# Kernel optimization log

Hardware: AMD Instinct MI355X
Metric: run time of the kernel (lower is better)

Reference implementation:

```python
import jax, jax.numpy as jnp
import numpy as np

IN_F, OUT_F = 4096, 4096
IN_Q, OUT_Q = IN_F // 4, OUT_F // 4


def setup_inputs() -> dict:
    key = jax.random.key(0)
    kx, kr, ki, kj, kk = jax.random.split(key, 5)
    std = 1.0 / np.sqrt(IN_F)
    x = jax.random.normal(kx, (4, 2048, IN_F), dtype=jnp.float32)
    Wr = std * jax.random.normal(kr, (OUT_Q, IN_Q), dtype=jnp.float32)
    Wi = std * jax.random.normal(ki, (OUT_Q, IN_Q), dtype=jnp.float32)
    Wj = std * jax.random.normal(kj, (OUT_Q, IN_Q), dtype=jnp.float32)
    Wk = std * jax.random.normal(kk, (OUT_Q, IN_Q), dtype=jnp.float32)
    bias = jnp.zeros((OUT_F,), dtype=jnp.float32)
    return {"x": x, "Wr": Wr, "Wi": Wi, "Wj": Wj, "Wk": Wk, "bias": bias}


def _hamilton_block(Wr, Wi, Wj, Wk):
    # Assemble the structured [4*out_q, 4*in_q] Hamilton block weight so the
    # whole op is ONE large GEMM instead of 16 small ones (same math).
    row_r = jnp.concatenate([Wr, -Wi, -Wj, -Wk], axis=1)
    row_i = jnp.concatenate([Wi,  Wr,  Wk, -Wj], axis=1)
    row_j = jnp.concatenate([Wj, -Wk,  Wr,  Wi], axis=1)
    row_k = jnp.concatenate([Wk,  Wj, -Wi,  Wr], axis=1)
    return jnp.concatenate([row_r, row_i, row_j, row_k], axis=0)  # [OUT_F, IN_F]


def reference(x, Wr, Wi, Wj, Wk, bias):
    W = _hamilton_block(Wr, Wi, Wj, Wk)
    # x: [B, S, IN_F] @ W.T -> [B, S, OUT_F]
    out = jnp.einsum('bsf,of->bso', x, W) + bias
    return out
```

## Files before the change

### kernel.cpp

```cpp
#include <hip/hip_runtime.h>
#include <hip/hip_bf16.h>


#define M_DIM 8192
#define N_DIM 4096
#define K_DIM 4096
#define BK 64
#define NT (K_DIM / BK)

typedef __attribute__((ext_vector_type(8))) short bf16x8;
typedef __attribute__((ext_vector_type(4))) float f32x4;
typedef __attribute__((ext_vector_type(8))) unsigned short ushort8;

static __device__ __forceinline__ unsigned short f2bf(float f) {
    unsigned int u = __float_as_uint(f);
    return (unsigned short)((u + 0x7fffu + ((u >> 16) & 1u)) >> 16);
}
static __device__ __forceinline__ unsigned short f2bf_sgn(float f, unsigned int sg) {
    unsigned int u = __float_as_uint(f) ^ sg;
    return (unsigned short)((u + 0x7fffu + ((u >> 16) & 1u)) >> 16);
}

__global__ __launch_bounds__(256) void cvt_x_kernel(const float* __restrict__ x,
                                                    unsigned short* __restrict__ xb) {
    int i = (blockIdx.x * 256 + threadIdx.x) * 8;
    f32x4 a = __builtin_nontemporal_load((const f32x4*)(x + i));
    f32x4 b = __builtin_nontemporal_load((const f32x4*)(x + i + 4));
    ushort8 o;
    o[0] = f2bf(a[0]); o[1] = f2bf(a[1]); o[2] = f2bf(a[2]); o[3] = f2bf(a[3]);
    o[4] = f2bf(b[0]); o[5] = f2bf(b[1]); o[6] = f2bf(b[2]); o[7] = f2bf(b[3]);
    *(ushort8*)(xb + i) = o;
}

__global__ __launch_bounds__(256) void prep_w_kernel(const float* __restrict__ Wr,
    const float* __restrict__ Wi, const float* __restrict__ Wj,
    const float* __restrict__ Wk, unsigned short* __restrict__ wb) {
    int row = blockIdx.x >> 1;
    int col = ((blockIdx.x & 1) * 256 + threadIdx.x) * 8;
    int p = row >> 10, q = col >> 10;
    int ci = p ^ q;
    const float* src = (ci == 0) ? Wr : (ci == 1) ? Wi : (ci == 2) ? Wj : Wk;
    unsigned int sg = ((0x428Eu >> (p * 4 + q)) & 1u) << 31;
    int so = (row & 1023) * 1024 + (col & 1023);
    f32x4 a = *(const f32x4*)(src + so);
    f32x4 b = *(const f32x4*)(src + so + 4);
    ushort8 o;
    o[0] = f2bf_sgn(a[0], sg); o[1] = f2bf_sgn(a[1], sg);
    o[2] = f2bf_sgn(a[2], sg); o[3] = f2bf_sgn(a[3], sg);
    o[4] = f2bf_sgn(b[0], sg); o[5] = f2bf_sgn(b[1], sg);
    o[6] = f2bf_sgn(b[2], sg); o[7] = f2bf_sgn(b[3], sg);
    *(ushort8*)(wb + row * 4096 + col) = o;
}

#define GLD16(gp, lp) __builtin_amdgcn_global_load_lds( \
    (const __attribute__((address_space(1))) void*)(gp), \
    (__attribute__((address_space(3))) void*)(lp), 16, 0, 0)

#define BAR() do { asm volatile("" ::: "memory"); \
                   __builtin_amdgcn_s_barrier(); \
                   asm volatile("" ::: "memory"); } while (0)
#define VM(n) asm volatile("s_waitcnt vmcnt(" #n ")" ::: "memory")

static __device__ __forceinline__ f32x4 MF(bf16x8 a, bf16x8 b, f32x4 c) {
    return __builtin_amdgcn_mfma_f32_16x16x32_bf16(a, b, c, 0, 0, 0);
}

__global__ __launch_bounds__(1024, 4) void qgemm_bf16(
    const unsigned short* __restrict__ A, const unsigned short* __restrict__ B,
    const float* __restrict__ bias, float* __restrict__ out)
{
    __shared__ __align__(16) unsigned short Lsh[2][2][256 * 64];

    int bid = blockIdx.x;
    int cpx = gridDim.x >> 3;
    int wg  = (bid & 7) * cpx + (bid >> 3);
    int brow = (wg >> 4) * 256;
    int bcol = (wg & 15) * 256;

    int tid   = threadIdx.x;
    int lane  = tid & 63;
    int wid   = tid >> 6;
    int wm    = wid >> 2;
    int wn    = wid & 3;
    int fr    = lane & 15;
    int fslot = lane >> 4;
    unsigned e = (unsigned)(fr & 7);

    const unsigned short* Ag = A + (size_t)brow * K_DIM;
    const unsigned short* Bg = B + (size_t)bcol * K_DIM;
    const char* LshB = (const char*)&Lsh[0][0][0];

    unsigned oA0 = (unsigned)wm * 8192u + (unsigned)fr * 128u
                 + ((((unsigned)fslot) ^ e) << 4);
    unsigned oA1 = oA0 ^ 64u;
    unsigned oB0 = 0x8000u + (unsigned)wn * 8192u + (unsigned)fr * 128u
                 + ((((unsigned)fslot) ^ e) << 4);
    unsigned oB1 = oB0 ^ 64u;

    f32x4 acc[4][4] = {};

    auto stage = [&](int buf, int ab, int t) {
        const unsigned short* g = (ab ? Bg : Ag) + t * BK;
        unsigned short* l = &Lsh[buf][ab][0];
        #pragma unroll
        for (int i = 0; i < 2; ++i) {
            int c = i * 1024 + tid;
            int r = c >> 3, s = c & 7;
            GLD16(g + (size_t)r * K_DIM + ((s ^ (r & 7)) << 3), l + (c << 3));
        }
    };
    auto RD = [&](unsigned off) -> bf16x8 {
        return *(const bf16x8*)(LshB + off);
    };

#define CLUSTER(mi)                                                           \
    do {                                                                      \
        bf16x8 a0 = RD(oA0 + (mi) * 2048u), a1 = RD(oA1 + (mi) * 2048u);      \
        __builtin_amdgcn_s_setprio(1);                                        \
        _Pragma("unroll")                                                     \
        for (int ni = 0; ni < 4; ++ni) acc[mi][ni] = MF(a0, bf0[ni], acc[mi][ni]); \
        _Pragma("unroll")                                                     \
        for (int ni = 0; ni < 4; ++ni) acc[mi][ni] = MF(a1, bf1[ni], acc[mi][ni]); \
        __builtin_amdgcn_s_setprio(0);                                        \
    } while (0)

    bf16x8 bf0[4], bf1[4];

    stage(0, 0, 0); stage(0, 1, 0); stage(1, 1, 1);
    VM(2); BAR();

    for (int t = 0; t < NT; ++t) {
        int buf = t & 1;

        if (t + 1 < NT) stage(buf ^ 1, 0, t + 1);
        #pragma unroll
        for (int ni = 0; ni < 4; ++ni) {
            bf0[ni] = RD(oB0 + (unsigned)(ni * 2048));
            bf1[ni] = RD(oB1 + (unsigned)(ni * 2048));
        }
        CLUSTER(0);
        BAR();

        if (t + 2 < NT) stage(buf, 1, t + 2);
        CLUSTER(1);
        CLUSTER(2);
        CLUSTER(3);

        if (t < NT - 2) { VM(2); } else { VM(0); }
        BAR();
        oA0 ^= 0x10000u; oA1 ^= 0x10000u; oB0 ^= 0x10000u; oB1 ^= 0x10000u;
    }
#undef CLUSTER

    int cr = (lane >> 4) << 2;
    int cc = lane & 15;
    #pragma unroll
    for (int ni = 0; ni < 4; ++ni) {
        int col = bcol + wn * 64 + ni * 16 + cc;
        float bv = bias[col];
        #pragma unroll
        for (int mi = 0; mi < 4; ++mi) {
            int r0 = brow + wm * 64 + mi * 16 + cr;
            #pragma unroll
            for (int r = 0; r < 4; ++r)
                __builtin_nontemporal_store(acc[mi][ni][r] + bv,
                                            &out[(size_t)(r0 + r) * N_DIM + col]);
        }
    }
}

#define FBM 128
#define FBN 128
#define FBK 64
__global__ __launch_bounds__(256) void qgemm_fb(const float* __restrict__ x,
    const float* __restrict__ Wr, const float* __restrict__ Wi,
    const float* __restrict__ Wj, const float* __restrict__ Wk,
    const float* __restrict__ bias, float* __restrict__ out)
{
    __shared__ unsigned short As[FBM * FBK];
    __shared__ unsigned short Bs[FBN * FBK];

    int bid = blockIdx.x;
    int cpx = gridDim.x >> 3;
    int wg = (bid & 7) * cpx + (bid >> 3);
    int brow = (wg >> 5) * FBM;
    int bcol = (wg & 31) * FBN;

    int tid = threadIdx.x;
    int lane = tid & 63;
    int wv = tid >> 6;
    int wm = (wv >> 1) << 6;
    int wn = (wv & 1) << 6;
    int fr = lane & 15;
    int fk = (lane >> 4) << 3;

    int p = bcol >> 10;
    f32x4 acc[4][4] = {};

    for (int kt = 0; kt < K_DIM / FBK; ++kt) {
        int k0 = kt * FBK;
        int q = k0 >> 10;
        int ci = p ^ q;
        const float* wsrc = (ci == 0) ? Wr : (ci == 1) ? Wi : (ci == 2) ? Wj : Wk;
        unsigned int sg = ((0x428Eu >> (p * 4 + q)) & 1u) << 31;

        __syncthreads();
        #pragma unroll
        for (int i = 0; i < 4; ++i) {
            int c = i * 256 + tid;
            int row = c >> 3, colo = (c & 7) << 3;
            const float* s = x + (size_t)(brow + row) * K_DIM + k0 + colo;
            float4 a = *(const float4*)s;
            float4 b = *(const float4*)(s + 4);
            ushort8 o;
            o[0] = f2bf(a.x); o[1] = f2bf(a.y); o[2] = f2bf(a.z); o[3] = f2bf(a.w);
            o[4] = f2bf(b.x); o[5] = f2bf(b.y); o[6] = f2bf(b.z); o[7] = f2bf(b.w);
            *(ushort8*)(&As[c << 3]) = o;
        }
        #pragma unroll
        for (int i = 0; i < 4; ++i) {
            int c = i * 256 + tid;
            int row = c >> 3, colo = (c & 7) << 3;
            const float* s = wsrc + ((bcol + row) & 1023) * 1024 + ((k0 + colo) & 1023);
            float4 a = *(const float4*)s;
            float4 b = *(const float4*)(s + 4);
            ushort8 o;
            o[0] = f2bf_sgn(a.x, sg); o[1] = f2bf_sgn(a.y, sg);
            o[2] = f2bf_sgn(a.z, sg); o[3] = f2bf_sgn(a.w, sg);
            o[4] = f2bf_sgn(b.x, sg); o[5] = f2bf_sgn(b.y, sg);
            o[6] = f2bf_sgn(b.z, sg); o[7] = f2bf_sgn(b.w, sg);
            *(ushort8*)(&Bs[c << 3]) = o;
        }
        __syncthreads();

        #pragma unroll
        for (int ks = 0; ks < 2; ++ks) {
            bf16x8 af[4], bfr[4];
            #pragma unroll
            for (int m = 0; m < 4; ++m)
                af[m] = *(const bf16x8*)(&As[(wm + m * 16 + fr) * FBK + ks * 32 + fk]);
            #pragma unroll
            for (int n = 0; n < 4; ++n)
                bfr[n] = *(const bf16x8*)(&Bs[(wn + n * 16 + fr) * FBK + ks * 32 + fk]);
            #pragma unroll
            for (int m = 0; m < 4; ++m)
                #pragma unroll
                for (int n = 0; n < 4; ++n)
                    acc[m][n] = __builtin_amdgcn_mfma_f32_16x16x32_bf16(
                        af[m], bfr[n], acc[m][n], 0, 0, 0);
        }
    }

    int cr = (lane >> 4) << 2;
    int cc = lane & 15;
    #pragma unroll
    for (int n = 0; n < 4; ++n) {
        int col = bcol + wn + n * 16 + cc;
        float bv = bias[col];
        #pragma unroll
        for (int m = 0; m < 4; ++m) {
            int r0 = brow + wm + m * 16 + cr;
            #pragma unroll
            for (int r = 0; r < 4; ++r)
                out[(size_t)(r0 + r) * N_DIM + col] = acc[m][n][r] + bv;
        }
    }
}

extern "C" void kernel_launch(void* const* d_in, const int* in_sizes, int n_in,
                              void* d_out, int out_size, void* d_ws, size_t ws_size,
                              hipStream_t stream) {
    const float* x    = (const float*)d_in[0];
    const float* Wr   = (const float*)d_in[1];
    const float* Wi   = (const float*)d_in[2];
    const float* Wj   = (const float*)d_in[3];
    const float* Wk   = (const float*)d_in[4];
    const float* bias = (const float*)d_in[5];
    float* out = (float*)d_out;

    const size_t xb_bytes = (size_t)M_DIM * K_DIM * 2;
    const size_t wb_bytes = (size_t)N_DIM * K_DIM * 2;

    if (ws_size >= xb_bytes + wb_bytes) {
        unsigned short* xb = (unsigned short*)d_ws;
        unsigned short* wb = (unsigned short*)((char*)d_ws + xb_bytes);
        cvt_x_kernel<<<(M_DIM * K_DIM) / 2048, 256, 0, stream>>>(x, xb);
        prep_w_kernel<<<N_DIM * 2, 256, 0, stream>>>(Wr, Wi, Wj, Wk, wb);
        const int n_blocks = (M_DIM / 256) * (N_DIM / 256);
        qgemm_bf16<<<n_blocks, 1024, 0, stream>>>(xb, wb, bias, out);
    } else {
        const int n_blocks = (M_DIM / FBM) * (N_DIM / FBN);
        qgemm_fb<<<n_blocks, 256, 0, stream>>>(x, Wr, Wi, Wj, Wk, bias, out);
    }
}
```

Measured before the change: 274.4 us.

## Restructure bf16 GEMM to 8 waves with 32x32x16 MFMA and k-slab LDS layout

Rewrites the main GEMM kernel to use 512 threads (8 waves, 2x4), each computing a 128x64 sub-tile with 32x32x16 bf16 MFMAs instead of 16x16x32. The LDS layout changes to k-slab-major staging with fixed offsets, and fragments are fetched through inline-asm ds_read_b128 with immediate offsets. A software-pipelined lgkmcnt schedule overlaps LDS reads with MFMAs. This raises per-wave data reuse and cuts LDS read traffic per FLOP. In exchange, A and B now share one double-buffered stage with a full vmcnt(0) wait each iteration, which may expose global-load latency, and the unswizzled layout risks LDS bank conflicts.

```diff
diff --git a/kernel.cpp b/kernel.cpp
--- a/kernel.cpp
+++ b/kernel.cpp
@@ -10,6 +10,7 @@
 
 typedef __attribute__((ext_vector_type(8))) short bf16x8;
 typedef __attribute__((ext_vector_type(4))) float f32x4;
+typedef __attribute__((ext_vector_type(16))) float f32x16;
 typedef __attribute__((ext_vector_type(8))) unsigned short ushort8;
 
 static __device__ __forceinline__ unsigned short f2bf(float f) {
@@ -59,17 +60,38 @@
 #define BAR() do { asm volatile("" ::: "memory"); \
                    __builtin_amdgcn_s_barrier(); \
                    asm volatile("" ::: "memory"); } while (0)
-#define VM(n) asm volatile("s_waitcnt vmcnt(" #n ")" ::: "memory")
-
-static __device__ __forceinline__ f32x4 MF(bf16x8 a, bf16x8 b, f32x4 c) {
-    return __builtin_amdgcn_mfma_f32_16x16x32_bf16(a, b, c, 0, 0, 0);
-}
-
-__global__ __launch_bounds__(1024, 4) void qgemm_bf16(
+#define VM0() asm volatile("s_waitcnt vmcnt(0)" ::: "memory")
+#define SB()  __builtin_amdgcn_sched_barrier(0)
+#define LGKM(n) do { asm volatile("s_waitcnt lgkmcnt(" #n ")" ::: "memory"); SB(); } while (0)
+
+#define DSR(dst, addr, imm) \
+    asm volatile("ds_read_b128 %0, %1 offset:" imm : "=v"(dst) : "v"(addr))
+
+#define MF32(a, b, c) __builtin_amdgcn_mfma_f32_32x32x16_bf16(a, b, c, 0, 0, 0)
+
+#define DECL6(F) bf16x8 F##a0, F##a1, F##a2, F##a3, F##b0, F##b1
+#define RD6(F, A0, A1, A2, A3, B0, B1) do { \
+    DSR(F##a0, vA, A0); DSR(F##a1, vA, A1); DSR(F##a2, vA, A2); DSR(F##a3, vA, A3); \
+    DSR(F##b0, vB, B0); DSR(F##b1, vB, B1); } while (0)
+
+#define MFMA8(F) do { \
+    __builtin_amdgcn_s_setprio(1); \
+    acc[0][0] = MF32(F##a0, F##b0, acc[0][0]); \
+    acc[0][1] = MF32(F##a0, F##b1, acc[0][1]); \
+    acc[1][0] = MF32(F##a1, F##b0, acc[1][0]); \
+    acc[1][1] = MF32(F##a1, F##b1, acc[1][1]); \
+    acc[2][0] = MF32(F##a2, F##b0, acc[2][0]); \
+    acc[2][1] = MF32(F##a2, F##b1, acc[2][1]); \
+    acc[3][0] = MF32(F##a3, F##b0, acc[3][0]); \
+    acc[3][1] = MF32(F##a3, F##b1, acc[3][1]); \
+    __builtin_amdgcn_s_setprio(0); \
+} while (0)
+
+__global__ __launch_bounds__(512, 2) void qgemm_bf16(
     const unsigned short* __restrict__ A, const unsigned short* __restrict__ B,
     const float* __restrict__ bias, float* __restrict__ out)
 {
-    __shared__ __align__(16) unsigned short Lsh[2][2][256 * 64];
+    __shared__ __align__(16) unsigned short Lsh[65536];
 
     int bid = blockIdx.x;
     int cpx = gridDim.x >> 3;
@@ -77,94 +99,80 @@
     int brow = (wg >> 4) * 256;
     int bcol = (wg & 15) * 256;
 
-    int tid   = threadIdx.x;
-    int lane  = tid & 63;
-    int wid   = tid >> 6;
-    int wm    = wid >> 2;
-    int wn    = wid & 3;
-    int fr    = lane & 15;
-    int fslot = lane >> 4;
-    unsigned e = (unsigned)(fr & 7);
+    int tid  = threadIdx.x;
+    int lane = tid & 63;
+    int wid  = tid >> 6;
+    int wm   = wid >> 2;
+    int wn   = wid & 3;
+    int l31  = lane & 31;
+    int hi   = lane >> 5;
 
     const unsigned short* Ag = A + (size_t)brow * K_DIM;
     const unsigned short* Bg = B + (size_t)bcol * K_DIM;
-    const char* LshB = (const char*)&Lsh[0][0][0];
-
-    unsigned oA0 = (unsigned)wm * 8192u + (unsigned)fr * 128u
-                 + ((((unsigned)fslot) ^ e) << 4);
-    unsigned oA1 = oA0 ^ 64u;
-    unsigned oB0 = 0x8000u + (unsigned)wn * 8192u + (unsigned)fr * 128u
-                 + ((((unsigned)fslot) ^ e) << 4);
-    unsigned oB1 = oB0 ^ 64u;
-
-    f32x4 acc[4][4] = {};
-
-    auto stage = [&](int buf, int ab, int t) {
-        const unsigned short* g = (ab ? Bg : Ag) + t * BK;
-        unsigned short* l = &Lsh[buf][ab][0];
-        #pragma unroll
-        for (int i = 0; i < 2; ++i) {
-            int c = i * 1024 + tid;
-            int r = c >> 3, s = c & 7;
-            GLD16(g + (size_t)r * K_DIM + ((s ^ (r & 7)) << 3), l + (c << 3));
-        }
+
+    unsigned lds0 = (unsigned)(size_t)(__attribute__((address_space(3))) void*)Lsh;
+    unsigned vA = lds0 + (unsigned)(wm * 4096 + l31 * 32 + hi * 16);
+    unsigned vB = lds0 + 32768u + (unsigned)(wn * 2048 + l31 * 32 + hi * 16);
+
+    int soff[4];
+    #pragma unroll
+    for (int i = 0; i < 4; ++i) {
+        int c = i * 512 + tid;
+        soff[i] = ((c >> 1) & 255) * 4096 + (c >> 9) * 16 + (c & 1) * 8;
+    }
+
+    f32x16 acc[4][2] = {};
+
+    auto STAGE = [&](int buf, int t) {
+        const unsigned short* ga = Ag + t * BK;
+        const unsigned short* gb = Bg + t * BK;
+        char* l = (char*)Lsh + buf * 65536;
+        #pragma unroll
+        for (int i = 0; i < 4; ++i)
+            GLD16(ga + soff[i], l + (i * 512 + tid) * 16);
+        #pragma unroll
+        for (int i = 0; i < 4; ++i)
+            GLD16(gb + soff[i], l + 32768 + (i * 512 + tid) * 16);
     };
-    auto RD = [&](unsigned off) -> bf16x8 {
-        return *(const bf16x8*)(LshB + off);
-    };
-
-#define CLUSTER(mi)                                                           \
-    do {                                                                      \
-        bf16x8 a0 = RD(oA0 + (mi) * 2048u), a1 = RD(oA1 + (mi) * 2048u);      \
-        __builtin_amdgcn_s_setprio(1);                                        \
-        _Pragma("unroll")                                                     \
-        for (int ni = 0; ni < 4; ++ni) acc[mi][ni] = MF(a0, bf0[ni], acc[mi][ni]); \
-        _Pragma("unroll")                                                     \
-        for (int ni = 0; ni < 4; ++ni) acc[mi][ni] = MF(a1, bf1[ni], acc[mi][ni]); \
-        __builtin_amdgcn_s_setprio(0);                                        \
-    } while (0)
-
-    bf16x8 bf0[4], bf1[4];
-
-    stage(0, 0, 0); stage(0, 1, 0); stage(1, 1, 1);
-    VM(2); BAR();
+
+    STAGE(0, 0);
+    VM0(); BAR();
 
     for (int t = 0; t < NT; ++t) {
-        int buf = t & 1;
-
-        if (t + 1 < NT) stage(buf ^ 1, 0, t + 1);
-        #pragma unroll
-        for (int ni = 0; ni < 4; ++ni) {
-            bf0[ni] = RD(oB0 + (unsigned)(ni * 2048));
-            bf1[ni] = RD(oB1 + (unsigned)(ni * 2048));
-        }
-        CLUSTER(0);
+        if (t + 1 < NT) STAGE((t & 1) ^ 1, t + 1);
+
+        DECL6(f0); DECL6(f1); DECL6(f2); DECL6(f3);
+        RD6(f0, "0", "1024", "2048", "3072", "0", "1024");
+        RD6(f1, "8192", "9216", "10240", "11264", "8192", "9216");
+        LGKM(6);
+        MFMA8(f0);
+        RD6(f2, "16384", "17408", "18432", "19456", "16384", "17408");
+        LGKM(6);
+        MFMA8(f1);
+        RD6(f3, "24576", "25600", "26624", "27648", "24576", "25600");
+        LGKM(6);
+        MFMA8(f2);
+        LGKM(0);
+        MFMA8(f3);
+
+        VM0();
         BAR();
-
-        if (t + 2 < NT) stage(buf, 1, t + 2);
-        CLUSTER(1);
-        CLUSTER(2);
-        CLUSTER(3);
-
-        if (t < NT - 2) { VM(2); } else { VM(0); }
-        BAR();
-        oA0 ^= 0x10000u; oA1 ^= 0x10000u; oB0 ^= 0x10000u; oB1 ^= 0x10000u;
-    }
-#undef CLUSTER
-
-    int cr = (lane >> 4) << 2;
-    int cc = lane & 15;
+        vA ^= 0x10000u; vB ^= 0x10000u;
+    }
+
     #pragma unroll
-    for (int ni = 0; ni < 4; ++ni) {
-        int col = bcol + wn * 64 + ni * 16 + cc;
+    for (int ni = 0; ni < 2; ++ni) {
+        int col = bcol + wn * 64 + ni * 32 + l31;
         float bv = bias[col];
         #pragma unroll
         for (int mi = 0; mi < 4; ++mi) {
-            int r0 = brow + wm * 64 + mi * 16 + cr;
-            #pragma unroll
-            for (int r = 0; r < 4; ++r)
+            int r0 = brow + wm * 128 + mi * 32 + 4 * hi;
+            #pragma unroll
+            for (int r = 0; r < 16; ++r) {
+                int row = r0 + (r & 3) + 8 * (r >> 2);
                 __builtin_nontemporal_store(acc[mi][ni][r] + bv,
-                                            &out[(size_t)(r0 + r) * N_DIM + col]);
+                                            &out[(size_t)row * N_DIM + col]);
+            }
         }
     }
 }
@@ -287,7 +295,7 @@
         cvt_x_kernel<<<(M_DIM * K_DIM) / 2048, 256, 0, stream>>>(x, xb);
         prep_w_kernel<<<N_DIM * 2, 256, 0, stream>>>(Wr, Wi, Wj, Wk, wb);
         const int n_blocks = (M_DIM / 256) * (N_DIM / 256);
-        qgemm_bf16<<<n_blocks, 1024, 0, stream>>>(xb, wb, bias, out);
+        qgemm_bf16<<<n_blocks, 512, 0, stream>>>(xb, wb, bias, out);
     } else {
         const int n_blocks = (M_DIM / FBM) * (N_DIM / FBN);
         qgemm_fb<<<n_blocks, 256, 0, stream>>>(x, Wr, Wi, Wj, Wk, bias, out);
```

Measured after the change: 311.0 us. +13.3%, slower.

## Restructure bf16 GEMM to 8 waves with 128x64 warp tiles and phased ping-pong pipeline

Applied to the files above, without the earlier changes.

The 256x256 GEMM tile is now computed by 512 threads (8 waves) instead of 1024, so each wave owns a 128x64 sub-tile with 32 accumulators. That doubles the MFMA work per LDS read of B. The main loop is unrolled by two K-steps into explicit phases. Each phase issues inline-asm ds_reads, splits global->LDS staging across the phases, and uses barriers, lgkmcnt/vmcnt waits and sched_barriers to interleave loads with MFMA clusters. The intent is more register-level reuse and finer overlap of memory with compute. The costs are higher register pressure, lower occupancy and more fragile manual scheduling.

```diff
diff --git a/kernel.cpp b/kernel.cpp
--- a/kernel.cpp
+++ b/kernel.cpp
@@ -7,6 +7,7 @@
 #define K_DIM 4096
 #define BK 64
 #define NT (K_DIM / BK)
+#define NIT (NT / 2)
 
 typedef __attribute__((ext_vector_type(8))) short bf16x8;
 typedef __attribute__((ext_vector_type(4))) float f32x4;
@@ -56,20 +57,47 @@
     (const __attribute__((address_space(1))) void*)(gp), \
     (__attribute__((address_space(3))) void*)(lp), 16, 0, 0)
 
-#define BAR() do { asm volatile("" ::: "memory"); \
-                   __builtin_amdgcn_s_barrier(); \
-                   asm volatile("" ::: "memory"); } while (0)
-#define VM(n) asm volatile("s_waitcnt vmcnt(" #n ")" ::: "memory")
-
-static __device__ __forceinline__ f32x4 MF(bf16x8 a, bf16x8 b, f32x4 c) {
-    return __builtin_amdgcn_mfma_f32_16x16x32_bf16(a, b, c, 0, 0, 0);
-}
-
-__global__ __launch_bounds__(1024, 4) void qgemm_bf16(
+#define SB()  __builtin_amdgcn_sched_barrier(0)
+#define DSR(dst, addr, imm) \
+    asm volatile("ds_read_b128 %0, %1 offset:" imm : "=v"(dst) : "v"(addr))
+#define MF(a, b, c) __builtin_amdgcn_mfma_f32_16x16x32_bf16(a, b, c, 0, 0, 0)
+
+#define RDB(B0, B1) do { \
+    DSR(b0k0, B0, "0"); DSR(b1k0, B0, "2048"); \
+    DSR(b2k0, B0, "4096"); DSR(b3k0, B0, "6144"); \
+    DSR(b0k1, B1, "0"); DSR(b1k1, B1, "2048"); \
+    DSR(b2k1, B1, "4096"); DSR(b3k1, B1, "6144"); } while (0)
+
+#define APHASE(A0, A1, I0, I1, ML, MH, WAITS, ...) do { \
+    bf16x8 xk0l, xk0h, xk1l, xk1h; \
+    DSR(xk0l, A0, I0); DSR(xk0h, A0, I1); \
+    DSR(xk1l, A1, I0); DSR(xk1h, A1, I1); \
+    __VA_ARGS__; \
+    __builtin_amdgcn_s_barrier(); \
+    asm volatile("s_waitcnt lgkmcnt(0)" ::: "memory"); SB(); \
+    __builtin_amdgcn_s_setprio(1); \
+    acc[ML][0] = MF(xk0l, b0k0, acc[ML][0]); acc[ML][1] = MF(xk0l, b1k0, acc[ML][1]); \
+    acc[ML][2] = MF(xk0l, b2k0, acc[ML][2]); acc[ML][3] = MF(xk0l, b3k0, acc[ML][3]); \
+    acc[MH][0] = MF(xk0h, b0k0, acc[MH][0]); acc[MH][1] = MF(xk0h, b1k0, acc[MH][1]); \
+    acc[MH][2] = MF(xk0h, b2k0, acc[MH][2]); acc[MH][3] = MF(xk0h, b3k0, acc[MH][3]); \
+    acc[ML][0] = MF(xk1l, b0k1, acc[ML][0]); acc[ML][1] = MF(xk1l, b1k1, acc[ML][1]); \
+    acc[ML][2] = MF(xk1l, b2k1, acc[ML][2]); acc[ML][3] = MF(xk1l, b3k1, acc[ML][3]); \
+    acc[MH][0] = MF(xk1h, b0k1, acc[MH][0]); acc[MH][1] = MF(xk1h, b1k1, acc[MH][1]); \
+    acc[MH][2] = MF(xk1h, b2k1, acc[MH][2]); acc[MH][3] = MF(xk1h, b3k1, acc[MH][3]); \
+    __builtin_amdgcn_s_setprio(0); \
+    WAITS; \
+    __builtin_amdgcn_s_barrier(); \
+} while (0)
+
+#define LGKM8() asm volatile("s_waitcnt lgkmcnt(8)" ::: "memory")
+#define VMW(n)  asm volatile("s_waitcnt vmcnt(" #n ")" ::: "memory")
+#define NOOP()  do {} while (0)
+
+__global__ __launch_bounds__(512, 2) void qgemm_bf16(
     const unsigned short* __restrict__ A, const unsigned short* __restrict__ B,
     const float* __restrict__ bias, float* __restrict__ out)
 {
-    __shared__ __align__(16) unsigned short Lsh[2][2][256 * 64];
+    __shared__ __align__(16) unsigned short Lsh[2][2][2][128 * 64];
 
     int bid = blockIdx.x;
     int cpx = gridDim.x >> 3;
@@ -80,7 +108,7 @@
     int tid   = threadIdx.x;
     int lane  = tid & 63;
     int wid   = tid >> 6;
-    int wm    = wid >> 2;
+    int hA    = wid >> 2;
     int wn    = wid & 3;
     int fr    = lane & 15;
     int fslot = lane >> 4;
@@ -88,69 +116,73 @@
 
     const unsigned short* Ag = A + (size_t)brow * K_DIM;
     const unsigned short* Bg = B + (size_t)bcol * K_DIM;
-    const char* LshB = (const char*)&Lsh[0][0][0];
-
-    unsigned oA0 = (unsigned)wm * 8192u + (unsigned)fr * 128u
-                 + ((((unsigned)fslot) ^ e) << 4);
-    unsigned oA1 = oA0 ^ 64u;
-    unsigned oB0 = 0x8000u + (unsigned)wn * 8192u + (unsigned)fr * 128u
-                 + ((((unsigned)fslot) ^ e) << 4);
-    unsigned oB1 = oB0 ^ 64u;
-
-    f32x4 acc[4][4] = {};
-
-    auto stage = [&](int buf, int ab, int t) {
-        const unsigned short* g = (ab ? Bg : Ag) + t * BK;
-        unsigned short* l = &Lsh[buf][ab][0];
-        #pragma unroll
-        for (int i = 0; i < 2; ++i) {
-            int c = i * 1024 + tid;
-            int r = c >> 3, s = c & 7;
-            GLD16(g + (size_t)r * K_DIM + ((s ^ (r & 7)) << 3), l + (c << 3));
-        }
+
+    unsigned lds0 = (unsigned)(size_t)(__attribute__((address_space(3))) void*)Lsh;
+    unsigned inrow = (((unsigned)fslot ^ e) << 4);
+    unsigned vA0e = lds0 + (unsigned)(hA * 16384 + fr * 128) + inrow;
+    unsigned vA1e = vA0e ^ 64u;
+    unsigned vA0o = vA0e + 65536u, vA1o = vA1e + 65536u;
+    unsigned vB0e = lds0 + 32768u
+                  + (unsigned)((wn >> 1) * 16384 + ((wn & 1) * 64 + fr) * 128) + inrow;
+    unsigned vB1e = vB0e ^ 64u;
+    unsigned vB0o = vB0e + 65536u, vB1o = vB1e + 65536u;
+
+    int soff0 = (tid >> 3) * K_DIM + (((tid & 7) ^ ((tid >> 3) & 7)) << 3);
+    int soff1 = soff0 + 64 * K_DIM;
+
+    f32x4 acc[8][4] = {};
+    bf16x8 b0k0, b1k0, b2k0, b3k0, b0k1, b1k1, b2k1, b3k1;
+
+    auto stgA = [&](int buf, int h, int t) {
+        const unsigned short* g = Ag + (size_t)(h * 128) * K_DIM + t * BK;
+        unsigned short* l = &Lsh[buf][0][h][0];
+        GLD16(g + soff0, l + tid * 8);
+        GLD16(g + soff1, l + 4096 + tid * 8);
     };
-    auto RD = [&](unsigned off) -> bf16x8 {
-        return *(const bf16x8*)(LshB + off);
+    auto stgB = [&](int buf, int h, int t) {
+        const unsigned short* g = Bg + (size_t)(h * 128) * K_DIM + t * BK;
+        unsigned short* l = &Lsh[buf][1][h][0];
+        GLD16(g + soff0, l + tid * 8);
+        GLD16(g + soff1, l + 4096 + tid * 8);
     };
 
-#define CLUSTER(mi)                                                           \
-    do {                                                                      \
-        bf16x8 a0 = RD(oA0 + (mi) * 2048u), a1 = RD(oA1 + (mi) * 2048u);      \
-        __builtin_amdgcn_s_setprio(1);                                        \
-        _Pragma("unroll")                                                     \
-        for (int ni = 0; ni < 4; ++ni) acc[mi][ni] = MF(a0, bf0[ni], acc[mi][ni]); \
-        _Pragma("unroll")                                                     \
-        for (int ni = 0; ni < 4; ++ni) acc[mi][ni] = MF(a1, bf1[ni], acc[mi][ni]); \
-        __builtin_amdgcn_s_setprio(0);                                        \
-    } while (0)
-
-    bf16x8 bf0[4], bf1[4];
-
-    stage(0, 0, 0); stage(0, 1, 0); stage(1, 1, 1);
-    VM(2); BAR();
-
-    for (int t = 0; t < NT; ++t) {
-        int buf = t & 1;
-
-        if (t + 1 < NT) stage(buf ^ 1, 0, t + 1);
-        #pragma unroll
-        for (int ni = 0; ni < 4; ++ni) {
-            bf0[ni] = RD(oB0 + (unsigned)(ni * 2048));
-            bf1[ni] = RD(oB1 + (unsigned)(ni * 2048));
-        }
-        CLUSTER(0);
-        BAR();
-
-        if (t + 2 < NT) stage(buf, 1, t + 2);
-        CLUSTER(1);
-        CLUSTER(2);
-        CLUSTER(3);
-
-        if (t < NT - 2) { VM(2); } else { VM(0); }
-        BAR();
-        oA0 ^= 0x10000u; oA1 ^= 0x10000u; oB0 ^= 0x10000u; oB1 ^= 0x10000u;
-    }
-#undef CLUSTER
+    stgA(0, 0, 0); stgA(0, 1, 0); stgB(0, 0, 0); stgB(0, 1, 0);
+    stgB(1, 0, 1); stgB(1, 1, 1);
+    VMW(4); SB();
+    __builtin_amdgcn_s_barrier();
+
+    for (int n = 0; n < NIT; ++n) {
+        int te = 2 * n + 2;
+        int to = 2 * n + 3;
+        bool g1 = (n + 1 < NIT);
+
+        RDB(vB0e, vB1e);
+        APHASE(vA0e, vA1e, "0", "2048", 0, 1, NOOP(),
+               stgA(1, 0, 2 * n + 1); LGKM8());
+        APHASE(vA0e, vA1e, "4096", "6144", 2, 3, NOOP(),
+               stgA(1, 1, 2 * n + 1); if (g1) stgB(0, 0, te));
+        APHASE(vA0e, vA1e, "8192", "10240", 4, 5, NOOP(),
+               if (g1) stgB(0, 1, te));
+        if (n < NIT - 1) {
+            APHASE(vA0e, vA1e, "12288", "14336", 6, 7, VMW(4), NOOP());
+        } else {
+            APHASE(vA0e, vA1e, "12288", "14336", 6, 7, VMW(0), NOOP());
+        }
+
+        RDB(vB0o, vB1o);
+        APHASE(vA0o, vA1o, "0", "2048", 0, 1, NOOP(),
+               if (g1) stgA(0, 0, te); LGKM8());
+        APHASE(vA0o, vA1o, "4096", "6144", 2, 3, NOOP(),
+               if (g1) stgA(0, 1, te));
+        APHASE(vA0o, vA1o, "8192", "10240", 4, 5, NOOP(),
+               if (g1) stgB(1, 0, to));
+        if (n < NIT - 1) {
+            APHASE(vA0o, vA1o, "12288", "14336", 6, 7, VMW(4),
+                   stgB(1, 1, to));
+        } else {
+            APHASE(vA0o, vA1o, "12288", "14336", 6, 7, VMW(0), NOOP());
+        }
+    }
 
     int cr = (lane >> 4) << 2;
     int cc = lane & 15;
@@ -159,8 +191,8 @@
         int col = bcol + wn * 64 + ni * 16 + cc;
         float bv = bias[col];
         #pragma unroll
-        for (int mi = 0; mi < 4; ++mi) {
-            int r0 = brow + wm * 64 + mi * 16 + cr;
+        for (int mi = 0; mi < 8; ++mi) {
+            int r0 = brow + hA * 128 + mi * 16 + cr;
             #pragma unroll
             for (int r = 0; r < 4; ++r)
                 __builtin_nontemporal_store(acc[mi][ni][r] + bv,
@@ -287,7 +319,7 @@
         cvt_x_kernel<<<(M_DIM * K_DIM) / 2048, 256, 0, stream>>>(x, xb);
         prep_w_kernel<<<N_DIM * 2, 256, 0, stream>>>(Wr, Wi, Wj, Wk, wb);
         const int n_blocks = (M_DIM / 256) * (N_DIM / 256);
-        qgemm_bf16<<<n_blocks, 1024, 0, stream>>>(xb, wb, bias, out);
+        qgemm_bf16<<<n_blocks, 512, 0, stream>>>(xb, wb, bias, out);
     } else {
         const int n_blocks = (M_DIM / FBM) * (N_DIM / FBN);
         qgemm_fb<<<n_blocks, 256, 0, stream>>>(x, Wr, Wi, Wj, Wk, bias, out);
```

Result: no change. 272.2 us (-0.8%).
